# Performance work log

Measured on AMD Instinct MI355X. Metric: run time of the kernel, lower is better.

Reference implementation:

```python
import jax, jax.numpy as jnp
import numpy as np
import math

N_ENTITIES = 200000
N_ITEMS = 100000
N_REL = 40
DIM = 64
N_HEADS = 2
DK = DIM // N_HEADS
N_EDGES = 1500000
K_EDGES = 256
K_ITEMS = 100


def setup_inputs() -> dict:
    key = jax.random.key(0)
    k1, k2, k3, k4, k5, k6 = jax.random.split(key, 6)
    entity_emb = jax.random.normal(k1, (N_ENTITIES, DIM), jnp.float32) * 0.1
    W_Q = jax.random.normal(k2, (DIM, DIM), jnp.float32) * (1.0 / math.sqrt(DIM))
    relation_emb = jax.random.normal(k3, (N_REL - 1, DIM), jnp.float32) * 0.1
    edge_index = jax.random.randint(k4, (2, N_EDGES), 0, N_ENTITIES, jnp.int32)
    # edge_type in [1, N_REL-1]: code indexes relation_emb[edge_type - 1]
    edge_type = jax.random.randint(k5, (N_EDGES,), 1, N_REL, jnp.int32)
    # uniform(0,1) driving the gumbel noise -log(-log(u)); clipped away from 0
    noise_u = jax.random.uniform(k6, (N_EDGES,), jnp.float32, 1e-9, 1.0)
    return {"entity_emb": entity_emb, "W_Q": W_Q, "relation_emb": relation_emb,
            "noise_u": noise_u, "edge_index": edge_index, "edge_type": edge_type}


def reference(entity_emb, W_Q, relation_emb, noise_u, edge_index, edge_type):
    head, tail = edge_index[0], edge_index[1]
    E = edge_index.shape[1]

    # --- norm_attn_computer (AttnHGCN): per-edge multi-head attention ---
    # project once on nodes, then gather (same math as (emb[head] @ W_Q))
    proj = entity_emb @ W_Q                               # [N, D]
    q = proj[head].reshape(E, N_HEADS, DK)                # [E, H, Dk]
    k = proj[tail].reshape(E, N_HEADS, DK)                # [E, H, Dk]
    rel = relation_emb[edge_type - 1].reshape(E, N_HEADS, DK)
    attn = jnp.sum(q * k * rel, axis=-1) / math.sqrt(DK)  # [E, H]
    edge_attn_logits = attn.mean(axis=-1)                 # [E]

    # scatter_softmax over head nodes, then multiply by head degree (norm)
    seg_max = jax.lax.stop_gradient(
        jax.ops.segment_max(edge_attn_logits, head, num_segments=N_ENTITIES))
    ex = jnp.exp(edge_attn_logits - seg_max[head])
    denom = jax.ops.segment_sum(ex, head, num_segments=N_ENTITIES)
    edge_attn_score = ex / denom[head]
    deg = jax.ops.segment_sum(jnp.ones_like(edge_attn_logits), head,
                              num_segments=N_ENTITIES)
    edge_attn_score = edge_attn_score * deg[head]         # [E]

    # --- attn logit sums per item (head + tail scatter_sum), topk 100 ---
    sum_by_node = (jax.ops.segment_sum(edge_attn_logits, head, num_segments=N_ENTITIES)
                   + jax.ops.segment_sum(edge_attn_logits, tail, num_segments=N_ENTITIES))
    top_items_v, top_attn_items = jax.lax.top_k(sum_by_node[:N_ITEMS], K_ITEMS)

    # --- gumbel-noise injection + edge topk 256 ---
    noisy_score = edge_attn_score + (-jnp.log(-jnp.log(noise_u)))
    topk_v, topk_attn_edge_id = jax.lax.top_k(noisy_score, K_EDGES)

    return (edge_attn_score, topk_v, topk_attn_edge_id, top_items_v, top_attn_items)
```

## Files before the change

### kernel.cpp

```cpp
#include <hip/hip_runtime.h>

#define N_ENTITIES 200000
#define N_ITEMS    100000
#define DIM        64
#define N_EDGES    1500000
#define K_EDGES    256
#define K_ITEMS    100
#define SCALE      0.08838834764831845f

#define CAND_CAP   8192
#define NBLK3      1024
#define NB1        256
#define EPB        5860
#define BSH        8
#define NBUCK      782
#define NSC        (NBUCK * NB1)
#define L2CAP      2816
#define PROJB      12500

typedef unsigned long long u64;


__device__ __forceinline__ unsigned fkey(float x) {
    unsigned u = __float_as_uint(x);
    return (u & 0x80000000u) ? ~u : (u | 0x80000000u);
}
__device__ __forceinline__ float funkey(unsigned k) {
    return (k & 0x80000000u) ? __uint_as_float(k & 0x7fffffffu)
                             : __uint_as_float(~k);
}

__device__ __forceinline__ unsigned select_digit(const unsigned* __restrict__ hist,
                                                 unsigned Keff, unsigned* above) {
    unsigned cum = 0;
    int b = 255;
    for (; b > 0; --b) {
        unsigned hb = hist[b];
        if (cum + hb >= Keff) break;
        cum += hb;
    }
    *above = cum;
    return (unsigned)b;
}

__global__ __launch_bounds__(256) void proj_bhist_kernel(const float* __restrict__ emb,
                                                         const float* __restrict__ W,
                                                         float* __restrict__ proj,
                                                         const int* __restrict__ head,
                                                         unsigned* __restrict__ off) {
    __shared__ float part[4][16][64];
    const int t = threadIdx.x;

    if (blockIdx.x >= PROJB) {
        unsigned* lh = (unsigned*)&part[0][0][0];
        const int vb = blockIdx.x - PROJB;
        for (int k = t; k < NBUCK; k += 256) lh[k] = 0;
        __syncthreads();
        int base = vb * EPB;
        int end = base + EPB; if (end > N_EDGES) end = N_EDGES;
        for (int e = base + t; e < end; e += 256)
            atomicAdd(&lh[(unsigned)head[e] >> BSH], 1u);
        __syncthreads();
        for (int k = t; k < NBUCK; k += 256)
            off[(size_t)k * NB1 + vb] = lh[k];
        return;
    }

    const int c = t & 63;
    const int q = __builtin_amdgcn_readfirstlane(t >> 6);

    float Wreg[16];
#pragma unroll
    for (int j = 0; j < 16; ++j) Wreg[j] = W[(q * 16 + j) * 64 + c];

    const int base = blockIdx.x * 16;
    const float* erow = emb + (size_t)base * 64 + q * 16;

    float acc[16];
#pragma unroll
    for (int r = 0; r < 16; ++r) acc[r] = 0.f;
#pragma unroll
    for (int r = 0; r < 16; ++r) {
#pragma unroll
        for (int j = 0; j < 16; ++j)
            acc[r] += erow[r * 64 + j] * Wreg[j];
    }
#pragma unroll
    for (int r = 0; r < 16; ++r) part[q][r][c] = acc[r];
    __syncthreads();
#pragma unroll
    for (int it = 0; it < 4; ++it) {
        int oi = t + it * 256;
        int r = oi >> 6, cc = oi & 63;
        float s = part[0][r][cc] + part[1][r][cc] + part[2][r][cc] + part[3][r][cc];
        proj[(size_t)(base + r) * 64 + cc] = s;
    }
}

__global__ void scanA_kernel(unsigned* __restrict__ a, unsigned* __restrict__ bsum) {
    __shared__ unsigned s[256];
    int t = threadIdx.x, i = blockIdx.x * 256 + t;
    unsigned v = a[i];
    s[t] = v;
    __syncthreads();
    for (int off = 1; off < 256; off <<= 1) {
        unsigned x = s[t];
        unsigned y = (t >= off) ? s[t - off] : 0u;
        __syncthreads();
        s[t] = x + y;
        __syncthreads();
    }
    a[i] = s[t] - v;
    if (t == 255) bsum[blockIdx.x] = s[t];
}
__global__ __launch_bounds__(256) void scanB_kernel(const unsigned* __restrict__ bsum,
                                                    unsigned* __restrict__ a) {
    __shared__ unsigned part[4];
    const int b = blockIdx.x;
    const int t = threadIdx.x;
    unsigned s = 0;
    for (int j = t; j < b; j += 256) s += bsum[j];
#pragma unroll
    for (int off = 1; off < 64; off <<= 1) s += __shfl_xor(s, off, 64);
    if ((t & 63) == 0) part[t >> 6] = s;
    __syncthreads();
    unsigned prefix = part[0] + part[1] + part[2] + part[3];
    a[b * 256 + t] += prefix;
}

__global__ __launch_bounds__(256) void bscat_kernel(const int* __restrict__ head,
                                                    const int* __restrict__ tail,
                                                    const int* __restrict__ etype,
                                                    const unsigned* __restrict__ off,
                                                    u64* __restrict__ rec2) {
    __shared__ unsigned lh[NBUCK];
    __shared__ unsigned loff[NBUCK];
    for (int k = threadIdx.x; k < NBUCK; k += 256) {
        lh[k] = 0;
        loff[k] = off[(size_t)k * NB1 + blockIdx.x];
    }
    __syncthreads();
    int base = blockIdx.x * EPB;
    int end = base + EPB; if (end > N_EDGES) end = N_EDGES;
    for (int e = base + threadIdx.x; e < end; e += 256) {
        unsigned h = (unsigned)head[e];
        unsigned bkt = h >> BSH;
        unsigned r = atomicAdd(&lh[bkt], 1u);
        u64 R = ((u64)h << 45) | ((u64)(unsigned)tail[e] << 27)
              | ((u64)(unsigned)(etype[e] - 1) << 21) | (u64)(unsigned)e;
        rec2[loff[bkt] + r] = R;
    }
}

__global__ __launch_bounds__(256) void csrnode_kernel(const u64* __restrict__ rec2,
                                                      const unsigned* __restrict__ off,
                                                      const float4* __restrict__ proj4,
                                                      const float4* __restrict__ rel4,
                                                      float* __restrict__ logits,
                                                      float2* __restrict__ nd,
                                                      float* __restrict__ sumhead,
                                                      float* __restrict__ sumI) {
    __shared__ u64 sdst[L2CAP];
    __shared__ unsigned short srank[L2CAP];
    __shared__ unsigned lh[256];
    __shared__ unsigned lscan[256];
    const int t = threadIdx.x;
    const int bkt = blockIdx.x;
    const unsigned gstart = off[(size_t)bkt * NB1];
    const unsigned gend = (bkt == NBUCK - 1) ? (unsigned)N_EDGES
                                             : off[(size_t)(bkt + 1) * NB1];
    unsigned n = gend - gstart;
    if (n > L2CAP) n = L2CAP;
    lh[t] = 0;
    __syncthreads();
    for (unsigned j = t; j < n; j += 256) {
        u64 R = rec2[gstart + j];
        unsigned hl = (unsigned)(R >> 45) & 255u;
        srank[j] = (unsigned short)atomicAdd(&lh[hl], 1u);
    }
    __syncthreads();
    unsigned v0 = lh[t];
    lscan[t] = v0;
    __syncthreads();
    for (int o = 1; o < 256; o <<= 1) {
        unsigned x = lscan[t];
        unsigned y = (t >= o) ? lscan[t - o] : 0u;
        __syncthreads();
        lscan[t] = x + y;
        __syncthreads();
    }
    unsigned excl = lscan[t] - v0;
    __syncthreads();
    lscan[t] = excl;
    __syncthreads();
    for (unsigned j = t; j < n; j += 256) {
        u64 R = rec2[gstart + j];
        unsigned hl = (unsigned)(R >> 45) & 255u;
        sdst[lscan[hl] + srank[j]] = R;
    }
    __syncthreads();

    const int lane = t & 63;
    const int wv = t >> 6;
    const int slot = lane >> 4, sl = lane & 15;
    for (int ln = 0; ln < 64; ++ln) {
        const int local = wv * 64 + ln;
        const int node = (bkt << BSH) + local;
        if (node >= N_ENTITIES) break;
        const unsigned s0 = lscan[local];
        const unsigned len = lh[local];
        float4 ph = proj4[(size_t)node * 16 + sl];
        float dsum = 0.f, lsum = 0.f;
        for (unsigned k0 = 0; k0 < len; k0 += 8) {
            unsigned ka = k0 + slot, kb = ka + 4;
            bool va = (ka < len), vb = (kb < len);
            u64 Ra = sdst[s0 + (va ? ka : 0u)];
            u64 Rb = sdst[s0 + (vb ? kb : 0u)];
            unsigned ta = (unsigned)(Ra >> 27) & 0x3FFFFu, ria = ((unsigned)(Ra >> 21)) & 63u;
            unsigned tb = (unsigned)(Rb >> 27) & 0x3FFFFu, rib = ((unsigned)(Rb >> 21)) & 63u;
            unsigned ea = (unsigned)Ra & 0x1FFFFFu, eb = (unsigned)Rb & 0x1FFFFFu;
            float4 pa = proj4[(size_t)ta * 16 + sl];
            float4 qa = rel4[(size_t)ria * 16 + sl];
            float4 pb = proj4[(size_t)tb * 16 + sl];
            float4 qb = rel4[(size_t)rib * 16 + sl];
            float xa = ph.x * pa.x * qa.x + ph.y * pa.y * qa.y
                     + ph.z * pa.z * qa.z + ph.w * pa.w * qa.w;
            float xb = ph.x * pb.x * qb.x + ph.y * pb.y * qb.y
                     + ph.z * pb.z * qb.z + ph.w * pb.w * qb.w;
            xa += __shfl_xor(xa, 1, 64);  xb += __shfl_xor(xb, 1, 64);
            xa += __shfl_xor(xa, 2, 64);  xb += __shfl_xor(xb, 2, 64);
            xa += __shfl_xor(xa, 4, 64);  xb += __shfl_xor(xb, 4, 64);
            xa += __shfl_xor(xa, 8, 64);  xb += __shfl_xor(xb, 8, 64);
            if (sl == 0) {
                if (va) {
                    float lg = xa * SCALE;
                    logits[ea] = lg;
                    dsum += __expf(lg);
                    lsum += lg;
                    if (ta < N_ITEMS) atomicAdd(&sumI[ta], lg);
                }
                if (vb) {
                    float lg = xb * SCALE;
                    logits[eb] = lg;
                    dsum += __expf(lg);
                    lsum += lg;
                    if (tb < N_ITEMS) atomicAdd(&sumI[tb], lg);
                }
            }
        }
        dsum += __shfl_xor(dsum, 16, 64);
        dsum += __shfl_xor(dsum, 32, 64);
        lsum += __shfl_xor(lsum, 16, 64);
        lsum += __shfl_xor(lsum, 32, 64);
        if (lane == 0) {
            nd[node] = make_float2(dsum, (float)len);
            sumhead[node] = lsum;
        }
    }
}

__global__ __launch_bounds__(256) void edge_pass3(const float* __restrict__ logits,
                           const int* __restrict__ head,
                           const float2* __restrict__ nd, const float* __restrict__ noise_u,
                           const float* __restrict__ sumhead, const float* __restrict__ sumI,
                           float* __restrict__ out_scores, unsigned* __restrict__ keysE,
                           unsigned* __restrict__ keysI, unsigned* __restrict__ hists) {
    __shared__ unsigned hh[512];
    for (int j = threadIdx.x; j < 512; j += blockDim.x) hh[j] = 0;
    __syncthreads();
    const int stride = NBLK3 * 256;
    for (int i = blockIdx.x * blockDim.x + threadIdx.x; i < N_EDGES; i += stride) {
        float lg = logits[i];
        float2 dd = nd[head[i]];
        float score = __expf(lg) / dd.x * dd.y;
        out_scores[i] = score;
        float noise = -logf(-logf(noise_u[i]));
        unsigned k = fkey(score + noise);
        keysE[i] = k;
        atomicAdd(&hh[k >> 24], 1u);
        if (i < N_ITEMS) {
            unsigned ki = fkey(sumhead[i] + sumI[i]);
            keysI[i] = ki;
            atomicAdd(&hh[256 + (ki >> 24)], 1u);
        }
    }
    __syncthreads();
    for (int j = threadIdx.x; j < 512; j += blockDim.x) {
        unsigned v = hh[j];
        if (v) atomicAdd(&hists[j], v);
    }
}

__global__ void collect_kernel(const unsigned* __restrict__ keysE,
                               const unsigned* __restrict__ keysI,
                               const unsigned* __restrict__ hists,
                               unsigned* __restrict__ counters, unsigned* __restrict__ cand) {
    const int y = blockIdx.y;
    const unsigned* keys = y ? keysI : keysE;
    const int n = y ? N_ITEMS : N_EDGES;
    const unsigned K = y ? K_ITEMS : K_EDGES;
    const unsigned* H = hists + (size_t)y * 256;
    unsigned aboveA;
    unsigned binA = select_digit(H, K, &aboveA);
    const unsigned T = binA << 24;
    unsigned* cd = cand + (size_t)y * 2 * CAND_CAP;

    int i = blockIdx.x * blockDim.x + threadIdx.x;
    int stride = gridDim.x * blockDim.x;
    for (; i < n; i += stride) {
        unsigned k = keys[i];
        if (k >= T) {
            unsigned p = atomicAdd(&counters[y], 1u);
            if (p < (unsigned)CAND_CAP) { cd[2 * p] = k; cd[2 * p + 1] = (unsigned)i; }
        }
    }
}

__global__ void final_topk_kernel(const unsigned* __restrict__ cand,
                                  const unsigned* __restrict__ counters,
                                  float* __restrict__ out_topkv, float* __restrict__ out_topki,
                                  float* __restrict__ out_itemv, float* __restrict__ out_itemi) {
    __shared__ unsigned sk[CAND_CAP];
    __shared__ unsigned si[CAND_CAP];
    const int y = blockIdx.x;
    const int K = y ? K_ITEMS : K_EDGES;
    float* outv = y ? out_itemv : out_topkv;
    float* outi = y ? out_itemi : out_topki;
    const unsigned* cd = cand + (size_t)y * 2 * CAND_CAP;
    unsigned m = counters[y];
    if (m > (unsigned)CAND_CAP) m = CAND_CAP;
    for (unsigned i = threadIdx.x; i < m; i += blockDim.x) {
        sk[i] = cd[2 * i];
        si[i] = cd[2 * i + 1];
    }
    __syncthreads();
    for (unsigned i = threadIdx.x; i < m; i += blockDim.x) {
        unsigned ki = sk[i], xi = si[i];
        int r = 0;
        for (unsigned j = 0; j < m; ++j) {
            unsigned kj = sk[j];
            if (kj > ki || (kj == ki && si[j] < xi)) r++;
        }
        if (r < K) {
            outv[r] = funkey(ki);
            outi[r] = (float)xi;
        }
    }
}

extern "C" void kernel_launch(void* const* d_in, const int* in_sizes, int n_in,
                              void* d_out, int out_size, void* d_ws, size_t ws_size,
                              hipStream_t stream) {
    (void)in_sizes; (void)n_in; (void)out_size; (void)ws_size;
    const float* emb    = (const float*)d_in[0];
    const float* W      = (const float*)d_in[1];
    const float* rel    = (const float*)d_in[2];
    const float* noise  = (const float*)d_in[3];
    const int*   eidx   = (const int*)d_in[4];
    const int*   etype  = (const int*)d_in[5];
    const int* head = eidx;
    const int* tail = eidx + N_EDGES;

    float* out        = (float*)d_out;
    float* out_scores = out;
    float* out_topkv  = out + N_EDGES;
    float* out_topki  = out + N_EDGES + K_EDGES;
    float* out_itemv  = out + N_EDGES + 2 * K_EDGES;
    float* out_itemi  = out + N_EDGES + 2 * K_EDGES + K_ITEMS;

    float* ws = (float*)d_ws;
    size_t o = 0;
    float*    proj    = ws + o;               o += (size_t)N_ENTITIES * DIM;
    unsigned* off     = (unsigned*)(ws + o);  o += NSC;
    unsigned* bsum    = (unsigned*)(ws + o);  o += 1024;
    u64*      rec2    = (u64*)(ws + o);       o += 2 * (size_t)N_EDGES;
    unsigned* keysE   = (unsigned*)rec2;
    unsigned* keysI   = keysE + N_EDGES;
    float*    logits  = ws + o;               o += N_EDGES;
    float2*   nd      = (float2*)(ws + o);    o += 2 * (size_t)N_ENTITIES;
    float*    sumhead = ws + o;               o += N_ENTITIES;
    float*    sumI    = ws + o;               o += N_ITEMS;
    unsigned* hists   = (unsigned*)(ws + o);  o += 512;
    unsigned* counters= (unsigned*)(ws + o);  o += 2;
    unsigned* cand    = (unsigned*)(ws + o);  o += 2 * 2 * CAND_CAP;

    hipMemsetAsync(sumI, 0, ((size_t)N_ITEMS + 512 + 2) * 4, stream);
    hipLaunchKernelGGL(proj_bhist_kernel, dim3(PROJB + NB1), dim3(256), 0, stream,
                       emb, W, proj, head, off);
    hipLaunchKernelGGL(scanA_kernel, dim3(NSC / 256), dim3(256), 0, stream, off, bsum);
    hipLaunchKernelGGL(scanB_kernel, dim3(NSC / 256), dim3(256), 0, stream, bsum, off);
    hipLaunchKernelGGL(bscat_kernel, dim3(NB1), dim3(256), 0, stream,
                       head, tail, etype, off, rec2);
    hipLaunchKernelGGL(csrnode_kernel, dim3(NBUCK), dim3(256), 0, stream,
                       rec2, off, (const float4*)proj, (const float4*)rel,
                       logits, nd, sumhead, sumI);
    hipLaunchKernelGGL(edge_pass3, dim3(NBLK3), dim3(256), 0, stream,
                       logits, head, nd, noise, sumhead, sumI,
                       out_scores, keysE, keysI, hists);
    hipLaunchKernelGGL(collect_kernel, dim3(512, 2), dim3(256), 0, stream,
                       keysE, keysI, hists, counters, cand);
    hipLaunchKernelGGL(final_topk_kernel, dim3(2), dim3(1024), 0, stream,
                       cand, counters, out_topkv, out_topki, out_itemv, out_itemi);
}
```

Before: 431.0 us.

## Split each csrnode bucket across four blocks of 64 nodes

Each 256-node bucket is now handled by four blocks, and each block keeps only the edges of its own 64-node quarter. That quadruples the grid from 782 to 3128 blocks and cuts shared memory per block from about 28KB to about 7KB, which should raise occupancy and parallelism. In exchange, every block reads the whole bucket's records twice, so global reads of rec2 go up fourfold. Per-quarter edges are capped at 768, and the in-node edge order now depends on atomics, so floating-point summation order can change.

Measured after the change: 421.9 us. 2.1% less time.

```diff
diff --git a/kernel.cpp b/kernel.cpp
--- a/kernel.cpp
+++ b/kernel.cpp
@@ -15,7 +15,8 @@
 #define BSH        8
 #define NBUCK      782
 #define NSC        (NBUCK * NB1)
-#define L2CAP      2816
+#define QSH        6
+#define QCAP       768
 #define PROJB      12500
 
 typedef unsigned long long u64;
@@ -160,52 +161,56 @@
                                                       float2* __restrict__ nd,
                                                       float* __restrict__ sumhead,
                                                       float* __restrict__ sumI) {
-    __shared__ u64 sdst[L2CAP];
-    __shared__ unsigned short srank[L2CAP];
-    __shared__ unsigned lh[256];
-    __shared__ unsigned lscan[256];
+    __shared__ u64 sdst[QCAP];
+    __shared__ unsigned lh[64];
+    __shared__ unsigned lscan[64];
+    __shared__ unsigned lcur[64];
     const int t = threadIdx.x;
-    const int bkt = blockIdx.x;
+    const int bkt = blockIdx.x >> 2;
+    const unsigned q = blockIdx.x & 3u;
     const unsigned gstart = off[(size_t)bkt * NB1];
     const unsigned gend = (bkt == NBUCK - 1) ? (unsigned)N_EDGES
                                              : off[(size_t)(bkt + 1) * NB1];
-    unsigned n = gend - gstart;
-    if (n > L2CAP) n = L2CAP;
-    lh[t] = 0;
+    const unsigned n = gend - gstart;
+    if (t < 64) lh[t] = 0;
+    __syncthreads();
+    for (unsigned j = t; j < n; j += 256) {
+        unsigned hl = (unsigned)(rec2[gstart + j] >> 45) & 255u;
+        if ((hl >> QSH) == q) atomicAdd(&lh[hl & 63u], 1u);
+    }
+    __syncthreads();
+    unsigned v0 = (t < 64) ? lh[t] : 0u;
+    if (t < 64) lscan[t] = v0;
+    __syncthreads();
+    for (int o = 1; o < 64; o <<= 1) {
+        unsigned x = 0, y = 0;
+        if (t < 64) { x = lscan[t]; y = (t >= o) ? lscan[t - o] : 0u; }
+        __syncthreads();
+        if (t < 64) lscan[t] = x + y;
+        __syncthreads();
+    }
+    if (t < 64) {
+        unsigned ex = lscan[t] - v0;
+        lscan[t] = ex;
+        lcur[t] = ex;
+    }
     __syncthreads();
     for (unsigned j = t; j < n; j += 256) {
         u64 R = rec2[gstart + j];
         unsigned hl = (unsigned)(R >> 45) & 255u;
-        srank[j] = (unsigned short)atomicAdd(&lh[hl], 1u);
-    }
-    __syncthreads();
-    unsigned v0 = lh[t];
-    lscan[t] = v0;
-    __syncthreads();
-    for (int o = 1; o < 256; o <<= 1) {
-        unsigned x = lscan[t];
-        unsigned y = (t >= o) ? lscan[t - o] : 0u;
-        __syncthreads();
-        lscan[t] = x + y;
-        __syncthreads();
-    }
-    unsigned excl = lscan[t] - v0;
-    __syncthreads();
-    lscan[t] = excl;
-    __syncthreads();
-    for (unsigned j = t; j < n; j += 256) {
-        u64 R = rec2[gstart + j];
-        unsigned hl = (unsigned)(R >> 45) & 255u;
-        sdst[lscan[hl] + srank[j]] = R;
+        if ((hl >> QSH) == q) {
+            unsigned d = atomicAdd(&lcur[hl & 63u], 1u);
+            if (d < QCAP) sdst[d] = R;
+        }
     }
     __syncthreads();
 
     const int lane = t & 63;
     const int wv = t >> 6;
     const int slot = lane >> 4, sl = lane & 15;
-    for (int ln = 0; ln < 64; ++ln) {
-        const int local = wv * 64 + ln;
-        const int node = (bkt << BSH) + local;
+    for (int ln = 0; ln < 16; ++ln) {
+        const int local = wv * 16 + ln;
+        const int node = (bkt << BSH) + ((int)q << QSH) + local;
         if (node >= N_ENTITIES) break;
         const unsigned s0 = lscan[local];
         const unsigned len = lh[local];
@@ -391,7 +396,7 @@
     hipLaunchKernelGGL(scanB_kernel, dim3(NSC / 256), dim3(256), 0, stream, bsum, off);
     hipLaunchKernelGGL(bscat_kernel, dim3(NB1), dim3(256), 0, stream,
                        head, tail, etype, off, rec2);
-    hipLaunchKernelGGL(csrnode_kernel, dim3(NBUCK), dim3(256), 0, stream,
+    hipLaunchKernelGGL(csrnode_kernel, dim3(NBUCK * 4), dim3(256), 0, stream,
                        rec2, off, (const float4*)proj, (const float4*)rel,
                        logits, nd, sumhead, sumI);
     hipLaunchKernelGGL(edge_pass3, dim3(NBLK3), dim3(256), 0, stream,
```
